# Performance work log

Measured on AMD Instinct MI355X. Metric: run time of the kernel, lower is better.

Reference implementation:

```python
import jax, jax.numpy as jnp
from jax import lax
import numpy as np

B, N, F = 256, 131072, 16


def _fir(x, h):
    """y[i] = x[i] + sum_{j=0}^{F-1} h[j] * x[i-j-1] for i >= F, else 0.

    x: (B, N) float, h: (F,) float. Implemented as one causal conv with an
    effective (F+1)-tap kernel k where k[0] = 1 (identity) and k[1:] = h.
    """
    f = h.shape[0]
    k = jnp.concatenate([jnp.ones((1,), dtype=h.dtype), h])          # (F+1,)
    # XLA conv is cross-correlation: out[i] = sum_d rhs[d] * lhs_pad[i+d].
    # With left-pad f and a reversed kernel, out[i] = sum_d k[d] * x[i-d].
    out = lax.conv_general_dilated(
        x[:, None, :],                        # (B, 1, N)
        k[::-1][None, None, :],               # (1, 1, F+1)
        window_strides=(1,),
        padding=[(f, 0)],
        dimension_numbers=("NCH", "OIH", "NCH"),
    )[:, 0, :]                                # (B, N)
    # Original code leaves y[i] = 0 for i < F.
    mask = jnp.arange(x.shape[-1]) >= f       # (N,)
    return jnp.where(mask, out, jnp.zeros((), dtype=x.dtype))


def setup_inputs() -> dict:
    key = jax.random.key(0)
    k1, k2 = jax.random.split(key)
    x = jax.random.normal(k1, (B, N), dtype=jnp.float32)
    # keras 'random_normal' initializer: stddev = 0.05
    kernel = jax.random.normal(k2, (1, F), dtype=jnp.float32) * 0.05
    return {"x": x, "kernel": kernel}


def reference(x, kernel):
    h = kernel[0]              # (F,) forward taps
    hr = h[::-1]               # reversed kernel (self.kernel_r)
    v = _fir(x, h)             # first deconv pass with kernel
    y = _fir(v, hr)            # second deconv pass with reversed kernel
    return y
```

## Files before the change

kernel.cpp:

```cpp
#include <hip/hip_runtime.h>


#define NROW 131072

__global__ void compute_g_kernel(const float* __restrict__ h, float* __restrict__ g) {
    int m = threadIdx.x;
    if (m < 33) {
        float s = 0.f;
        for (int a = 0; a <= 16; ++a) {
            int b = m - a;
            if (b < 0 || b > 16) continue;
            float ka = (a == 0) ? 1.f : h[a - 1];
            float kb = (b == 0) ? 1.f : h[16 - b];
            s += ka * kb;
        }
        g[m] = s;
    }
}

__global__ __launch_bounds__(256) void fir2_kernel(const float* __restrict__ x,
                                                   const float* __restrict__ h,
                                                   const float* __restrict__ g,
                                                   float* __restrict__ y) {
    const int bid = blockIdx.x;
    const int row = bid >> 5;
    const int chunk = bid & 31;
    const int i0 = chunk * 4096 + (int)threadIdx.x * 16;
    const float* __restrict__ xr = x + (size_t)row * NROW;
    float* __restrict__ yr = y + (size_t)row * NROW;

    float w[48];
#pragma unroll
    for (int k = 0; k < 12; ++k) {
        const int idx = i0 - 32 + 4 * k;
        float4 val;
        if (idx >= 0) val = *(const float4*)(xr + idx);
        else          val = make_float4(0.f, 0.f, 0.f, 0.f);
        w[4 * k + 0] = val.x; w[4 * k + 1] = val.y;
        w[4 * k + 2] = val.z; w[4 * k + 3] = val.w;
    }

    float o[16];
    if (i0 >= 32) {
        float gg[33];
#pragma unroll
        for (int m = 0; m < 33; ++m) gg[m] = g[m];
#pragma unroll
        for (int c = 0; c < 16; ++c) {
            float s = 0.f;
#pragma unroll
            for (int m = 0; m < 33; ++m) s += gg[m] * w[c + 32 - m];
            o[c] = s;
        }
    } else if (i0 == 0) {
#pragma unroll
        for (int c = 0; c < 16; ++c) o[c] = 0.f;
    } else {
        float hh[16];
#pragma unroll
        for (int j = 0; j < 16; ++j) hh[j] = h[j];
        float v[16];
#pragma unroll
        for (int u = 0; u < 16; ++u) {
            const int p = 16 + u;
            float s = w[p + 16];
#pragma unroll
            for (int j = 0; j < 16; ++j) s += hh[j] * w[p + 15 - j];
            v[u] = s;
        }
#pragma unroll
        for (int u = 0; u < 16; ++u) {
            float s = v[u];
#pragma unroll
            for (int j = 0; j < 16; ++j) {
                if (j <= u - 1) s += hh[15 - j] * v[u - 1 - j];
            }
            o[u] = s;
        }
    }

#pragma unroll
    for (int k = 0; k < 4; ++k) {
        float4 val = make_float4(o[4 * k + 0], o[4 * k + 1],
                                 o[4 * k + 2], o[4 * k + 3]);
        *(float4*)(yr + i0 + 4 * k) = val;
    }
}

extern "C" void kernel_launch(void* const* d_in, const int* in_sizes, int n_in,
                              void* d_out, int out_size, void* d_ws, size_t ws_size,
                              hipStream_t stream) {
    const float* x = (const float*)d_in[0];
    const float* h = (const float*)d_in[1];
    float* y = (float*)d_out;
    float* g = (float*)d_ws;

    compute_g_kernel<<<1, 64, 0, stream>>>(h, g);
    fir2_kernel<<<8192, 256, 0, stream>>>(x, h, g, y);
}
```

Baseline: 262.6 us.

## Shrink per-thread output to four samples for coalesced loads and lower registers

Each thread now computes 4 consecutive outputs instead of 16, so adjacent lanes read adjacent float4s rather than 64-byte-strided ones, and the grid grows fourfold. Register pressure drops (40-float window, 4 accumulators), which raises occupancy. The cost is more redundant halo loads per output, relying on cache, and a runtime-indexed boundary path for the first few outputs.

Result: slower. 362.7 us (+38.1%).

```diff
diff --git a/kernel.cpp b/kernel.cpp
--- a/kernel.cpp
+++ b/kernel.cpp
@@ -23,67 +23,78 @@
                                                    const float* __restrict__ g,
                                                    float* __restrict__ y) {
     const int bid = blockIdx.x;
-    const int row = bid >> 5;
-    const int chunk = bid & 31;
-    const int i0 = chunk * 4096 + (int)threadIdx.x * 16;
+    const int row = bid >> 7;
+    const int cid = ((bid & 127) << 8) + (int)threadIdx.x;
+    const int o0 = cid << 2;
     const float* __restrict__ xr = x + (size_t)row * NROW;
     float* __restrict__ yr = y + (size_t)row * NROW;
 
-    float w[48];
+    float gg[33];
 #pragma unroll
-    for (int k = 0; k < 12; ++k) {
-        const int idx = i0 - 32 + 4 * k;
-        float4 val;
-        if (idx >= 0) val = *(const float4*)(xr + idx);
-        else          val = make_float4(0.f, 0.f, 0.f, 0.f);
-        w[4 * k + 0] = val.x; w[4 * k + 1] = val.y;
-        w[4 * k + 2] = val.z; w[4 * k + 3] = val.w;
-    }
+    for (int m = 0; m < 33; ++m) gg[m] = g[m];
 
-    float o[16];
-    if (i0 >= 32) {
-        float gg[33];
+    float w[40];
+
+    if (bid & 127) {
 #pragma unroll
-        for (int m = 0; m < 33; ++m) gg[m] = g[m];
+        for (int k = 0; k < 10; ++k) {
+            float4 v = *(const float4*)(xr + (o0 - 36 + 4 * k));
+            w[4 * k + 0] = v.x; w[4 * k + 1] = v.y;
+            w[4 * k + 2] = v.z; w[4 * k + 3] = v.w;
+        }
+        float o[4];
 #pragma unroll
-        for (int c = 0; c < 16; ++c) {
+        for (int c = 0; c < 4; ++c) {
             float s = 0.f;
 #pragma unroll
-            for (int m = 0; m < 33; ++m) s += gg[m] * w[c + 32 - m];
+            for (int m = 0; m < 33; ++m) s += gg[m] * w[36 + c - m];
             o[c] = s;
         }
-    } else if (i0 == 0) {
+        *(float4*)(yr + o0) = make_float4(o[0], o[1], o[2], o[3]);
+    } else {
 #pragma unroll
-        for (int c = 0; c < 16; ++c) o[c] = 0.f;
-    } else {
-        float hh[16];
+        for (int k = 0; k < 10; ++k) {
+            const int ck = cid - 9 + k;
+            float4 v;
+            if (ck >= 0) v = *(const float4*)(xr + 4 * ck);
+            else         v = make_float4(0.f, 0.f, 0.f, 0.f);
+            w[4 * k + 0] = v.x; w[4 * k + 1] = v.y;
+            w[4 * k + 2] = v.z; w[4 * k + 3] = v.w;
+        }
+        float o[4];
+        if (cid >= 8) {
 #pragma unroll
-        for (int j = 0; j < 16; ++j) hh[j] = h[j];
-        float v[16];
+            for (int c = 0; c < 4; ++c) {
+                float s = 0.f;
 #pragma unroll
-        for (int u = 0; u < 16; ++u) {
-            const int p = 16 + u;
-            float s = w[p + 16];
-#pragma unroll
-            for (int j = 0; j < 16; ++j) s += hh[j] * w[p + 15 - j];
-            v[u] = s;
+                for (int m = 0; m < 33; ++m) s += gg[m] * w[36 + c - m];
+                o[c] = s;
+            }
+        } else if (cid < 4) {
+            o[0] = o[1] = o[2] = o[3] = 0.f;
+        } else {
+            float hh[16];
+            for (int j = 0; j < 16; ++j) hh[j] = h[j];
+            const int umax = o0 + 3 - 16;
+            float vv[16];
+            for (int u = 0; u <= umax; ++u) {
+                const int p = 16 + u;
+                float s = w[p - o0 + 36];
+                for (int j = 0; j < 16; ++j)
+                    s += hh[j] * w[p - 1 - j - o0 + 36];
+                vv[u] = s;
+            }
+            for (int c = 0; c < 4; ++c) {
+                const int i = o0 + c;
+                float s = vv[i - 16];
+                for (int j = 0; j < 16; ++j) {
+                    const int idx = i - 1 - j;
+                    if (idx >= 16) s += hh[15 - j] * vv[idx - 16];
+                }
+                o[c] = s;
+            }
         }
-#pragma unroll
-        for (int u = 0; u < 16; ++u) {
-            float s = v[u];
-#pragma unroll
-            for (int j = 0; j < 16; ++j) {
-                if (j <= u - 1) s += hh[15 - j] * v[u - 1 - j];
-            }
-            o[u] = s;
-        }
-    }
-
-#pragma unroll
-    for (int k = 0; k < 4; ++k) {
-        float4 val = make_float4(o[4 * k + 0], o[4 * k + 1],
-                                 o[4 * k + 2], o[4 * k + 3]);
-        *(float4*)(yr + i0 + 4 * k) = val;
+        *(float4*)(yr + o0) = make_float4(o[0], o[1], o[2], o[3]);
     }
 }
 
@@ -96,5 +107,5 @@
     float* g = (float*)d_ws;
 
     compute_g_kernel<<<1, 64, 0, stream>>>(h, g);
-    fir2_kernel<<<8192, 256, 0, stream>>>(x, h, g, y);
+    fir2_kernel<<<32768, 256, 0, stream>>>(x, h, g, y);
 }
```
